# Performance work log

Measured on AMD Instinct MI355X. Metric: run time of the kernel, lower is better.

## Reference

```python
import jax, jax.numpy as jnp
import numpy as np

B, S, C, D, K = 8, 1024, 8192, 256, 512
FREEDOM = 0.1

def setup_inputs() -> dict:
    key = jax.random.key(0)
    k1, k2, k3 = jax.random.split(key, 3)
    concept_seq = jax.random.uniform(k1, (B, S, C), dtype=jnp.float32)
    concept_emb = jax.random.uniform(k2, (C, D), dtype=jnp.float32)  # nn.Parameter(torch.rand(max_c+1, d_model))
    centroid_emb = jax.random.uniform(k3, (K, D), dtype=jnp.float32)
    return {"concept_seq": concept_seq, "concept_emb": concept_emb,
            "centroid_emb": centroid_emb, "domain": 0}

def reference(concept_seq, concept_emb, centroid_emb, domain):
    # normalize multi-hot rows by their count (rows summing to 0 use count=1)
    cnt = jnp.sum(concept_seq, axis=-1, keepdims=True)
    cnt = jnp.where(cnt == 0, jnp.ones_like(cnt), cnt)
    cs = concept_seq / cnt
    # weighted embedding sum: [B,S,C] @ [C,D] -> [B,S,D]
    e_free = jnp.einsum('bsc,cd->bsd', cs, concept_emb)
    # nearest centroid (argmin of cdist == argmin of squared distance)
    flat = e_free.reshape(-1, D)                               # [B*S, D]
    d2 = (jnp.sum(flat * flat, axis=1, keepdims=True)
          - 2.0 * flat @ centroid_emb.T
          + jnp.sum(centroid_emb * centroid_emb, axis=1))      # [B*S, K]
    idx = jnp.argmin(d2, axis=1)                               # [B*S]
    e_cent = centroid_emb[idx].reshape(e_free.shape)           # [B,S,D]
    return e_free * FREEDOM + e_cent * (1.0 - FREEDOM)
```

## Files before the change

### kernel.cpp

```cpp
#include <hip/hip_runtime.h>


typedef unsigned short u16;
typedef unsigned int   u32;
using bf16x8 = __attribute__((ext_vector_type(8))) short;
using f32x4  = __attribute__((ext_vector_type(4))) float;

#define MFMA_B16(A,B,C) __builtin_amdgcn_mfma_f32_16x16x32_bf16((A),(B),(C),0,0,0)

#define NSPLIT 4

static __device__ __forceinline__ u16 f2bf(float f){
  u32 u = __builtin_bit_cast(u32, f);
  u += 0x7FFFu + ((u >> 16) & 1u);
  return (u16)(u >> 16);
}
static __device__ __forceinline__ u16 f2bf_fast(float f){
  u32 u = __builtin_bit_cast(u32, f);
  return (u16)((u + 0x8000u) >> 16);
}
static __device__ __forceinline__ float bf2f(u16 h){
  u32 u = ((u32)h) << 16;
  return __builtin_bit_cast(float, u);
}
static __device__ __forceinline__ void split2(float va, float vb, u32& hw, u32& lw){
  u16 ha = f2bf(va), hb = f2bf(vb);
  hw = (u32)ha | ((u32)hb << 16);
  lw = (u32)f2bf(va - bf2f(ha)) | ((u32)f2bf(vb - bf2f(hb)) << 16);
}
static __device__ __forceinline__ void split2f(float va, float vb, u32& hw, u32& lw){
  u16 ha = f2bf_fast(va), hb = f2bf_fast(vb);
  hw = (u32)ha | ((u32)hb << 16);
  lw = (u32)f2bf_fast(va - bf2f(ha)) | ((u32)f2bf_fast(vb - bf2f(hb)) << 16);
}

#define SZ_PART    ((size_t)NSPLIT*8192UL*256UL*4UL)
#define OFF_CNT    (SZ_PART)
#define SZ_CNT     ((size_t)NSPLIT*8192UL*4UL)
#define OFF_BHI    (OFF_CNT + SZ_CNT)
#define SZ_BHI     (8192UL*256UL*2UL)
#define OFF_BLO    (OFF_BHI + SZ_BHI)
#define OFF_CTHI   (OFF_BLO + SZ_BHI)
#define SZ_CT      (512UL*256UL*2UL)
#define OFF_CTLO   (OFF_CTHI + SZ_CT)
#define OFF_CNORM  (OFF_CTLO + SZ_CT)

__global__ __launch_bounds__(256) void ce_prep(
    const float* __restrict__ emb, const float* __restrict__ cent,
    u16* __restrict__ Bhi, u16* __restrict__ Blo,
    u16* __restrict__ CThi, u16* __restrict__ CTlo,
    double* __restrict__ cnormd)
{
  const int b = blockIdx.x, t = threadIdx.x;
  const int l = t & 63;
  const int lr = l & 15, lk = l >> 4;
  if (b < 1024) {
    const int g  = b * 4 + (t >> 6);
    const int nt = g >> 8, ksg = g & 255;
    u32 hw[4], lw[4];
    #pragma unroll
    for (int p = 0; p < 4; ++p) {
      float va = emb[(size_t)(ksg*32 + lk*8 + 2*p    )*256 + nt*16 + lr];
      float vb = emb[(size_t)(ksg*32 + lk*8 + 2*p + 1)*256 + nt*16 + lr];
      split2(va, vb, hw[p], lw[p]);
    }
    const size_t fi = ((size_t)nt*256 + ksg)*64 + l;
    *(uint4*)(Bhi + fi*8) = make_uint4(hw[0],hw[1],hw[2],hw[3]);
    *(uint4*)(Blo + fi*8) = make_uint4(lw[0],lw[1],lw[2],lw[3]);
  } else if (b < 1088) {
    const int g  = (b - 1024) * 4 + (t >> 6);
    const int nt = g >> 3, ksg = g & 7;
    u32 hw[4], lw[4];
    #pragma unroll
    for (int p = 0; p < 4; ++p) {
      float va = cent[(size_t)(nt*16 + lr)*256 + ksg*32 + lk*8 + 2*p    ] - 0.5f;
      float vb = cent[(size_t)(nt*16 + lr)*256 + ksg*32 + lk*8 + 2*p + 1] - 0.5f;
      split2(va, vb, hw[p], lw[p]);
    }
    const size_t fi = ((size_t)nt*8 + ksg)*64 + l;
    *(uint4*)(CThi + fi*8) = make_uint4(hw[0],hw[1],hw[2],hw[3]);
    *(uint4*)(CTlo + fi*8) = make_uint4(lw[0],lw[1],lw[2],lw[3]);
  } else {
    const int row = (b - 1088)*8 + (t >> 5);
    const int h = t & 31;
    double s = 0.0;
    #pragma unroll
    for (int j = 0; j < 8; ++j) {
      float x = cent[(size_t)row*256 + h*8 + j] - 0.5f;
      s += (double)x * (double)x;
    }
    #pragma unroll
    for (int off = 16; off > 0; off >>= 1) s += __shfl_xor(s, off);
    if (h == 0) cnormd[row] = s;
  }
}

__global__ __launch_bounds__(512, 4) void ce_gemm(
    const float* __restrict__ seq,
    const u16* __restrict__ Bhi, const u16* __restrict__ Blo,
    float* __restrict__ part, float* __restrict__ cntpart)
{
  __shared__ char Ah[2][64*256];
  __shared__ char Al[2][64*256];

  const int t   = threadIdx.x;
  const int blk = blockIdx.x;
  const int mt  = blk >> 2;
  const int ks  = blk & 3;
  const size_t rowBase = (size_t)mt * 64;
  const int ar  = t >> 3;
  const int ac  = t & 7;
  const float* aptr = seq + (rowBase + ar) * 8192 + (size_t)ks * 2048 + ac * 16;

  const int w = t >> 6, l = t & 63;
  const int lr = l & 15, lk = l >> 4;

  f32x4 acc[4][2];
  #pragma unroll
  for (int i = 0; i < 4; ++i)
    #pragma unroll
    for (int j = 0; j < 2; ++j) acc[i][j] = (f32x4){0.f,0.f,0.f,0.f};

  float csum = 0.f;
  float4 areg[4];

  auto loadA = [&](void) {
    #pragma unroll
    for (int i = 0; i < 4; ++i) areg[i] = *(const float4*)(aptr + i*4);
  };
  auto stage8 = [&](int buf, int j) {
    const float4 A = areg[2*j], B = areg[2*j+1];
    float v[8] = {A.x, A.y, A.z, A.w, B.x, B.y, B.z, B.w};
    #pragma unroll
    for (int i = 0; i < 8; ++i) csum += v[i];
    u32 hw[4], lw[4];
    #pragma unroll
    for (int p = 0; p < 4; ++p) split2f(v[2*p], v[2*p+1], hw[p], lw[p]);
    const int slot = ac*2 + j;
    const int off  = ar*256 + ((slot ^ (ar & 7)) << 4);
    *(uint4*)(Ah[buf] + off) = make_uint4(hw[0],hw[1],hw[2],hw[3]);
    *(uint4*)(Al[buf] + off) = make_uint4(lw[0],lw[1],lw[2],lw[3]);
  };

  bf16x8 bhA[2], blA[2], bhB[2], blB[2];
  auto loadB_A = [&](int ksg) {
    #pragma unroll
    for (int ni = 0; ni < 2; ++ni) {
      const size_t fi = (((size_t)(w*2 + ni))*256 + ksg)*64 + l;
      bhA[ni] = *(const bf16x8*)(Bhi + fi*8);
      blA[ni] = *(const bf16x8*)(Blo + fi*8);
    }
  };
  auto loadB_B = [&](int ksg) {
    #pragma unroll
    for (int ni = 0; ni < 2; ++ni) {
      const size_t fi = (((size_t)(w*2 + ni))*256 + ksg)*64 + l;
      bhB[ni] = *(const bf16x8*)(Bhi + fi*8);
      blB[ni] = *(const bf16x8*)(Blo + fi*8);
    }
  };
  auto mfma_cluster = [&](int buf, int ksub, int sel) {
    bf16x8 ah[4], alo[4];
    #pragma unroll
    for (int mi = 0; mi < 4; ++mi) {
      const int row = mi*16 + lr;
      const int off = row*256 + (((ksub*4 + lk) ^ (row & 7)) << 4);
      ah[mi]  = *(const bf16x8*)(Ah[buf] + off);
      alo[mi] = *(const bf16x8*)(Al[buf] + off);
    }
    #pragma unroll
    for (int mi = 0; mi < 4; ++mi)
      #pragma unroll
      for (int ni = 0; ni < 2; ++ni) {
        const bf16x8 bh = sel ? bhB[ni] : bhA[ni];
        const bf16x8 bl = sel ? blB[ni] : blA[ni];
        acc[mi][ni] = MFMA_B16(ah[mi], bh, acc[mi][ni]);
        acc[mi][ni] = MFMA_B16(alo[mi], bh, acc[mi][ni]);
        acc[mi][ni] = MFMA_B16(ah[mi], bl, acc[mi][ni]);
      }
  };

  loadA();
  stage8(0, 0);
  stage8(0, 1);
  aptr += 128;
  loadA();
  loadB_A(ks*64 + 0);
  __syncthreads();

  for (int step = 0; step < 16; ++step) {
    const int cur = step & 1;
    const int ksg0 = ks*64 + step*4;
    const bool more = (step < 15);

    loadB_B(ksg0 + 1);
    if (more) stage8(cur^1, 0);
    mfma_cluster(cur, 0, 0);

    loadB_A(ksg0 + 2);
    if (more) stage8(cur^1, 1);
    mfma_cluster(cur, 1, 1);

    loadB_B(ksg0 + 3);
    if (step < 14) { aptr += 128; loadA(); }
    mfma_cluster(cur, 2, 0);

    if (more) loadB_A(ksg0 + 4);
    mfma_cluster(cur, 3, 1);

    __syncthreads();
  }

  {
    float c = csum;
    c += __shfl_xor(c, 1);
    c += __shfl_xor(c, 2);
    c += __shfl_xor(c, 4);
    if (ac == 0) cntpart[(size_t)ks*8192 + rowBase + ar] = c;
  }
  float* pbase = part + ((size_t)ks*8192 + rowBase)*256;
  #pragma unroll
  for (int mi = 0; mi < 4; ++mi)
    #pragma unroll
    for (int ni = 0; ni < 2; ++ni) {
      const int col = w*32 + ni*16 + lr;
      #pragma unroll
      for (int rr = 0; rr < 4; ++rr) {
        const int row = mi*16 + lk*4 + rr;
        pbase[(size_t)row*256 + col] = acc[mi][ni][rr];
      }
    }
}

__global__ __launch_bounds__(256) void ce_cent(
    const float* __restrict__ part, const float* __restrict__ cntpart,
    const u16* __restrict__ CThi, const u16* __restrict__ CTlo,
    const double* __restrict__ cnormd, const float* __restrict__ cent,
    float* __restrict__ out)
{
  __shared__ float eL[32][256];
  __shared__ char Eh[32*512];
  __shared__ char El[32*512];
  __shared__ float GL[32][512];
  __shared__ float cntL[32];
  __shared__ float enred[32][8];
  __shared__ float enL[32];

  const int t = threadIdx.x;
  const size_t rb = (size_t)blockIdx.x * 32;
  const int r  = t >> 3;
  const int c0 = (t & 7) * 32;

  if (t < 32) {
    float s = 0.f;
    #pragma unroll
    for (int p = 0; p < NSPLIT; ++p) s += cntpart[(size_t)p*8192 + rb + t];
    cntL[t] = (s == 0.f) ? 1.f : s;
  }
  __syncthreads();
  const float inv = 1.0f / cntL[r];
  float en = 0.f;
  #pragma unroll
  for (int jp = 0; jp < 4; ++jp) {
    float e8[8];
    #pragma unroll
    for (int q = 0; q < 2; ++q) {
      const float* p0 = part + (rb + r)*256 + c0 + jp*8 + q*4;
      float4 e4 = {0.f, 0.f, 0.f, 0.f};
      #pragma unroll
      for (int p = 0; p < NSPLIT; ++p) {
        float4 s0 = *(const float4*)(p0 + (size_t)p*2097152);
        e4.x += s0.x; e4.y += s0.y; e4.z += s0.z; e4.w += s0.w;
      }
      e4.x *= inv; e4.y *= inv; e4.z *= inv; e4.w *= inv;
      *(float4*)&eL[r][c0 + jp*8 + q*4] = e4;
      e8[q*4+0] = e4.x; e8[q*4+1] = e4.y; e8[q*4+2] = e4.z; e8[q*4+3] = e4.w;
    }
    u32 hw[4], lw[4];
    #pragma unroll
    for (int p = 0; p < 4; ++p) {
      float va = e8[2*p] - 0.5f, vb = e8[2*p+1] - 0.5f;
      split2(va, vb, hw[p], lw[p]);
      en += va*va + vb*vb;
    }
    const int slot = (t & 7)*4 + jp;
    const int off  = r*512 + ((slot ^ (r & 7)) << 4);
    *(uint4*)(Eh + off) = make_uint4(hw[0],hw[1],hw[2],hw[3]);
    *(uint4*)(El + off) = make_uint4(lw[0],lw[1],lw[2],lw[3]);
  }
  enred[r][t & 7] = en;
  __syncthreads();
  if (t < 32) {
    float s = 0.f;
    #pragma unroll
    for (int j = 0; j < 8; ++j) s += enred[t][j];
    enL[t] = s;
  }
  const int w = t >> 6, l = t & 63, lr = l & 15, lk = l >> 4;
  f32x4 acc[2][8];
  #pragma unroll
  for (int i = 0; i < 2; ++i)
    #pragma unroll
    for (int j = 0; j < 8; ++j) acc[i][j] = (f32x4){0.f,0.f,0.f,0.f};
  #pragma unroll
  for (int ksub = 0; ksub < 8; ++ksub) {
    bf16x8 ah[2], alo[2];
    #pragma unroll
    for (int mi = 0; mi < 2; ++mi) {
      const int row = mi*16 + lr;
      const int off = row*512 + (((ksub*4 + lk) ^ (row & 7)) << 4);
      ah[mi]  = *(const bf16x8*)(Eh + off);
      alo[mi] = *(const bf16x8*)(El + off);
    }
    bf16x8 bh[8], bl[8];
    #pragma unroll
    for (int ni = 0; ni < 8; ++ni) {
      const size_t fi = (((size_t)(w*8 + ni))*8 + ksub)*64 + l;
      bh[ni] = *(const bf16x8*)(CThi + fi*8);
      bl[ni] = *(const bf16x8*)(CTlo + fi*8);
    }
    #pragma unroll
    for (int mi = 0; mi < 2; ++mi)
      #pragma unroll
      for (int ni = 0; ni < 8; ++ni) {
        acc[mi][ni] = MFMA_B16(ah[mi],  bh[ni], acc[mi][ni]);
        acc[mi][ni] = MFMA_B16(alo[mi], bh[ni], acc[mi][ni]);
        acc[mi][ni] = MFMA_B16(ah[mi],  bl[ni], acc[mi][ni]);
      }
  }
  #pragma unroll
  for (int mi = 0; mi < 2; ++mi)
    #pragma unroll
    for (int ni = 0; ni < 8; ++ni)
      #pragma unroll
      for (int rr = 0; rr < 4; ++rr)
        GL[mi*16 + lk*4 + rr][w*128 + ni*16 + lr] = acc[mi][ni][rr];
  __syncthreads();
  for (int i = 0; i < 8; ++i) {
    const int row = w*8 + i;
    const double en_ = (double)enL[row];
    double best = 1e300; int bk = 0;
    #pragma unroll
    for (int jj = 0; jj < 8; ++jj) {
      const int k = jj*64 + l;
      const double d2 = en_ + cnormd[k] - 2.0*(double)GL[row][k];
      if (d2 < best) { best = d2; bk = k; }
    }
    #pragma unroll
    for (int off = 32; off > 0; off >>= 1) {
      const double ov = __shfl_xor(best, off);
      const int   ok = __shfl_xor(bk, off);
      if (ov < best || (ov == best && ok < bk)) { best = ov; bk = ok; }
    }
    const float* crow = cent + (size_t)bk*256;
    float4 ef = *(const float4*)&eL[row][l*4];
    float4 cf = *(const float4*)(crow + l*4);
    float4 o;
    o.x = 0.1f*ef.x + 0.9f*cf.x;
    o.y = 0.1f*ef.y + 0.9f*cf.y;
    o.z = 0.1f*ef.z + 0.9f*cf.z;
    o.w = 0.1f*ef.w + 0.9f*cf.w;
    *(float4*)(out + (rb + row)*256 + l*4) = o;
  }
}

extern "C" void kernel_launch(void* const* d_in, const int* in_sizes, int n_in,
                              void* d_out, int out_size, void* d_ws, size_t ws_size,
                              hipStream_t stream) {
  const float* seq  = (const float*)d_in[0];
  const float* emb  = (const float*)d_in[1];
  const float* cent = (const float*)d_in[2];
  float* out = (float*)d_out;
  char* ws = (char*)d_ws;

  float*  part    = (float*) (ws);
  float*  cntpart = (float*) (ws + OFF_CNT);
  u16*    Bhi     = (u16*)   (ws + OFF_BHI);
  u16*    Blo     = (u16*)   (ws + OFF_BLO);
  u16*    CThi    = (u16*)   (ws + OFF_CTHI);
  u16*    CTlo    = (u16*)   (ws + OFF_CTLO);
  double* cnormd  = (double*)(ws + OFF_CNORM);

  hipLaunchKernelGGL(ce_prep, dim3(1152), dim3(256), 0, stream,
                     emb, cent, Bhi, Blo, CThi, CTlo, cnormd);
  hipLaunchKernelGGL(ce_gemm, dim3(512), dim3(512), 0, stream,
                     seq, Bhi, Blo, part, cntpart);
  hipLaunchKernelGGL(ce_cent, dim3(256), dim3(256), 0, stream,
                     part, cntpart, CThi, CTlo, cnormd, cent, out);
}
```

Baseline: 148.4 us.

## Switch main GEMM to 32x32x16 MFMA with repacked B and LDS layout

Replaces the 16x16x32 bf16 MFMA tiling in the concept GEMM with 32x32x16 MFMAs, with each wave computing two 32x32 tiles. The B fragment prep layout, the LDS A layout and swizzle, the k-loop schedule and the output write mapping are all reworked to match. It also raises wave priority around the MFMA clusters. The aim is fewer B loads per FLOP and higher MFMA throughput, at the cost of a more complex swizzle, a different register footprint and more, smaller B loads per step.

```diff
diff --git a/kernel.cpp b/kernel.cpp
--- a/kernel.cpp
+++ b/kernel.cpp
@@ -5,10 +5,13 @@
 typedef unsigned int   u32;
 using bf16x8 = __attribute__((ext_vector_type(8))) short;
 using f32x4  = __attribute__((ext_vector_type(4))) float;
+using f32x16 = __attribute__((ext_vector_type(16))) float;
 
 #define MFMA_B16(A,B,C) __builtin_amdgcn_mfma_f32_16x16x32_bf16((A),(B),(C),0,0,0)
+#define MFMA32(A,B,C)   __builtin_amdgcn_mfma_f32_32x32x16_bf16((A),(B),(C),0,0,0)
 
 #define NSPLIT 4
+#define SWZ(r) ((((r)&7) ^ (((r)>>3)&3)))
 
 static __device__ __forceinline__ u16 f2bf(float f){
   u32 u = __builtin_bit_cast(u32, f);
@@ -53,21 +56,23 @@
 {
   const int b = blockIdx.x, t = threadIdx.x;
   const int l = t & 63;
-  const int lr = l & 15, lk = l >> 4;
   if (b < 1024) {
     const int g  = b * 4 + (t >> 6);
-    const int nt = g >> 8, ksg = g & 255;
+    const int nt = g >> 9, ksg = g & 511;
+    const int col = nt*32 + (l & 31);
+    const int k0  = ksg*16 + (l >> 5)*8;
     u32 hw[4], lw[4];
     #pragma unroll
     for (int p = 0; p < 4; ++p) {
-      float va = emb[(size_t)(ksg*32 + lk*8 + 2*p    )*256 + nt*16 + lr];
-      float vb = emb[(size_t)(ksg*32 + lk*8 + 2*p + 1)*256 + nt*16 + lr];
+      float va = emb[(size_t)(k0 + 2*p    )*256 + col];
+      float vb = emb[(size_t)(k0 + 2*p + 1)*256 + col];
       split2(va, vb, hw[p], lw[p]);
     }
-    const size_t fi = ((size_t)nt*256 + ksg)*64 + l;
+    const size_t fi = ((size_t)nt*512 + ksg)*64 + l;
     *(uint4*)(Bhi + fi*8) = make_uint4(hw[0],hw[1],hw[2],hw[3]);
     *(uint4*)(Blo + fi*8) = make_uint4(lw[0],lw[1],lw[2],lw[3]);
   } else if (b < 1088) {
+    const int lr = l & 15, lk = l >> 4;
     const int g  = (b - 1024) * 4 + (t >> 6);
     const int nt = g >> 3, ksg = g & 7;
     u32 hw[4], lw[4];
@@ -100,8 +105,8 @@
     const u16* __restrict__ Bhi, const u16* __restrict__ Blo,
     float* __restrict__ part, float* __restrict__ cntpart)
 {
-  __shared__ char Ah[2][64*256];
-  __shared__ char Al[2][64*256];
+  __shared__ char Ah[2][2*64*128];
+  __shared__ char Al[2][2*64*128];
 
   const int t   = threadIdx.x;
   const int blk = blockIdx.x;
@@ -113,13 +118,11 @@
   const float* aptr = seq + (rowBase + ar) * 8192 + (size_t)ks * 2048 + ac * 16;
 
   const int w = t >> 6, l = t & 63;
-  const int lr = l & 15, lk = l >> 4;
-
-  f32x4 acc[4][2];
-  #pragma unroll
-  for (int i = 0; i < 4; ++i)
-    #pragma unroll
-    for (int j = 0; j < 2; ++j) acc[i][j] = (f32x4){0.f,0.f,0.f,0.f};
+  const int lrow = l & 31, lhi = l >> 5;
+
+  f32x16 acc0 = {0.f}, acc1 = {0.f};
+  #pragma unroll
+  for (int i = 0; i < 16; ++i) { acc0[i] = 0.f; acc1[i] = 0.f; }
 
   float csum = 0.f;
   float4 areg[4];
@@ -136,48 +139,45 @@
     u32 hw[4], lw[4];
     #pragma unroll
     for (int p = 0; p < 4; ++p) split2f(v[2*p], v[2*p+1], hw[p], lw[p]);
-    const int slot = ac*2 + j;
-    const int off  = ar*256 + ((slot ^ (ar & 7)) << 4);
+    const int slot = ((ac & 3) << 1) | j;
+    const int off  = (ac >> 2)*8192 + ar*128 + ((slot ^ SWZ(ar)) << 4);
     *(uint4*)(Ah[buf] + off) = make_uint4(hw[0],hw[1],hw[2],hw[3]);
     *(uint4*)(Al[buf] + off) = make_uint4(lw[0],lw[1],lw[2],lw[3]);
   };
 
-  bf16x8 bhA[2], blA[2], bhB[2], blB[2];
+  bf16x8 bhA, blA, bhB, blB;
   auto loadB_A = [&](int ksg) {
-    #pragma unroll
-    for (int ni = 0; ni < 2; ++ni) {
-      const size_t fi = (((size_t)(w*2 + ni))*256 + ksg)*64 + l;
-      bhA[ni] = *(const bf16x8*)(Bhi + fi*8);
-      blA[ni] = *(const bf16x8*)(Blo + fi*8);
-    }
+    const size_t fi = (((size_t)w*512 + ksg)*64 + l)*8;
+    bhA = *(const bf16x8*)(Bhi + fi);
+    blA = *(const bf16x8*)(Blo + fi);
   };
   auto loadB_B = [&](int ksg) {
-    #pragma unroll
-    for (int ni = 0; ni < 2; ++ni) {
-      const size_t fi = (((size_t)(w*2 + ni))*256 + ksg)*64 + l;
-      bhB[ni] = *(const bf16x8*)(Bhi + fi*8);
-      blB[ni] = *(const bf16x8*)(Blo + fi*8);
-    }
-  };
-  auto mfma_cluster = [&](int buf, int ksub, int sel) {
-    bf16x8 ah[4], alo[4];
-    #pragma unroll
-    for (int mi = 0; mi < 4; ++mi) {
-      const int row = mi*16 + lr;
-      const int off = row*256 + (((ksub*4 + lk) ^ (row & 7)) << 4);
-      ah[mi]  = *(const bf16x8*)(Ah[buf] + off);
-      alo[mi] = *(const bf16x8*)(Al[buf] + off);
-    }
-    #pragma unroll
-    for (int mi = 0; mi < 4; ++mi)
-      #pragma unroll
-      for (int ni = 0; ni < 2; ++ni) {
-        const bf16x8 bh = sel ? bhB[ni] : bhA[ni];
-        const bf16x8 bl = sel ? blB[ni] : blA[ni];
-        acc[mi][ni] = MFMA_B16(ah[mi], bh, acc[mi][ni]);
-        acc[mi][ni] = MFMA_B16(alo[mi], bh, acc[mi][ni]);
-        acc[mi][ni] = MFMA_B16(ah[mi], bl, acc[mi][ni]);
-      }
+    const size_t fi = (((size_t)w*512 + ksg)*64 + l)*8;
+    bhB = *(const bf16x8*)(Bhi + fi);
+    blB = *(const bf16x8*)(Blo + fi);
+  };
+  auto cluster = [&](int buf, int ksub, bf16x8 bh, bf16x8 bl) {
+    const int khalf = ksub >> 2;
+    const int slot  = ((ksub & 3) << 1) | lhi;
+    bf16x8 ah0, al0, ah1, al1;
+    {
+      const int r0 = lrow;
+      const int o0 = khalf*8192 + r0*128 + ((slot ^ SWZ(r0)) << 4);
+      ah0 = *(const bf16x8*)(Ah[buf] + o0);
+      al0 = *(const bf16x8*)(Al[buf] + o0);
+      const int r1 = 32 + lrow;
+      const int o1 = khalf*8192 + r1*128 + ((slot ^ SWZ(r1)) << 4);
+      ah1 = *(const bf16x8*)(Ah[buf] + o1);
+      al1 = *(const bf16x8*)(Al[buf] + o1);
+    }
+    __builtin_amdgcn_s_setprio(1);
+    acc0 = MFMA32(ah0, bh, acc0);
+    acc1 = MFMA32(ah1, bh, acc1);
+    acc0 = MFMA32(al0, bh, acc0);
+    acc1 = MFMA32(al1, bh, acc1);
+    acc0 = MFMA32(ah0, bl, acc0);
+    acc1 = MFMA32(ah1, bl, acc1);
+    __builtin_amdgcn_s_setprio(0);
   };
 
   loadA();
@@ -185,28 +185,40 @@
   stage8(0, 1);
   aptr += 128;
   loadA();
-  loadB_A(ks*64 + 0);
+  loadB_A(ks*128 + 0);
   __syncthreads();
 
   for (int step = 0; step < 16; ++step) {
     const int cur = step & 1;
-    const int ksg0 = ks*64 + step*4;
+    const int kb  = ks*128 + step*8;
     const bool more = (step < 15);
 
-    loadB_B(ksg0 + 1);
+    loadB_B(kb + 1);
     if (more) stage8(cur^1, 0);
-    mfma_cluster(cur, 0, 0);
-
-    loadB_A(ksg0 + 2);
+    cluster(cur, 0, bhA, blA);
+
+    loadB_A(kb + 2);
+    cluster(cur, 1, bhB, blB);
+
+    loadB_B(kb + 3);
     if (more) stage8(cur^1, 1);
-    mfma_cluster(cur, 1, 1);
-
-    loadB_B(ksg0 + 3);
+    cluster(cur, 2, bhA, blA);
+
+    loadB_A(kb + 4);
+    cluster(cur, 3, bhB, blB);
+
+    loadB_B(kb + 5);
     if (step < 14) { aptr += 128; loadA(); }
-    mfma_cluster(cur, 2, 0);
-
-    if (more) loadB_A(ksg0 + 4);
-    mfma_cluster(cur, 3, 1);
+    cluster(cur, 4, bhA, blA);
+
+    loadB_A(kb + 6);
+    cluster(cur, 5, bhB, blB);
+
+    loadB_B(kb + 7);
+    cluster(cur, 6, bhA, blA);
+
+    if (more) loadB_A(kb + 8);
+    cluster(cur, 7, bhB, blB);
 
     __syncthreads();
   }
@@ -219,17 +231,13 @@
     if (ac == 0) cntpart[(size_t)ks*8192 + rowBase + ar] = c;
   }
   float* pbase = part + ((size_t)ks*8192 + rowBase)*256;
-  #pragma unroll
-  for (int mi = 0; mi < 4; ++mi)
-    #pragma unroll
-    for (int ni = 0; ni < 2; ++ni) {
-      const int col = w*32 + ni*16 + lr;
-      #pragma unroll
-      for (int rr = 0; rr < 4; ++rr) {
-        const int row = mi*16 + lk*4 + rr;
-        pbase[(size_t)row*256 + col] = acc[mi][ni][rr];
-      }
-    }
+  const int col = w*32 + lrow;
+  #pragma unroll
+  for (int reg = 0; reg < 16; ++reg) {
+    const int rsub = (reg & 3) + 8*(reg >> 2) + 4*lhi;
+    pbase[(size_t)(rsub     )*256 + col] = acc0[reg];
+    pbase[(size_t)(rsub + 32)*256 + col] = acc1[reg];
+  }
 }
 
 __global__ __launch_bounds__(256) void ce_cent(
```

New measurement: 143.4 us. 1.04x faster.
